# Kernel tuning notes

Hardware: AMD Instinct MI355X
Metric: run time of the kernel (lower is better)

Reference implementation:

```python
import jax, jax.numpy as jnp
import numpy as np

B, D, K = 4096, 768, 60


def setup_inputs() -> dict:
    key = jax.random.key(0)
    k1, k2, k3 = jax.random.split(key, 3)
    user_emb = jax.random.normal(k1, (B, D), dtype=jnp.float32)
    pos_item_emb = jax.random.normal(k2, (B, D), dtype=jnp.float32)
    # Per-row negative indices into the in-batch item table, excluding the
    # row's own positive (emulates the exclusion/sampling done on host in torch).
    r = jax.random.randint(k3, (B, K), 0, B, dtype=jnp.int32)
    rows = jnp.arange(B, dtype=jnp.int32)[:, None]
    neg_indices = jnp.where(r == rows, (r + 1) % B, r)
    return {"user_emb": user_emb, "pos_item_emb": pos_item_emb,
            "neg_indices": neg_indices}


def reference(user_emb, pos_item_emb, neg_indices):
    # u2i contrastive loss: logits = [u.pos, u.neg_1..neg_K], label 0, mean CE.
    logits_pos = jnp.sum(user_emb * pos_item_emb, axis=-1)          # (B,)
    neg_embs = pos_item_emb[neg_indices]                            # (B, K, D)
    logits_neg = jnp.einsum('bd,bkd->bk', user_emb, neg_embs)      # (B, K)
    logits = jnp.concatenate([logits_pos[:, None], logits_neg], axis=1)
    loss = -jax.nn.log_softmax(logits, axis=-1)[:, 0]               # label = 0
    return jnp.mean(loss)
```

## Files before the change

### kernel.cpp

```cpp
#include <hip/hip_runtime.h>
#include <hip/hip_fp16.h>
#include <math.h>


#define NB 4096
#define ND 768
#define NK 60
#define ND4  (ND / 4)
#define NDU  (ND / 2)
#define NLOGITS (NK + 1)
#define NPAD 64

#define NSLOT 64

#define WS_ITEMS_OFF 0
#define WS_USER_OFF  ((size_t)NB * ND * 2)
#define WS_SLOTS_OFF (WS_USER_OFF + (size_t)NB * ND * 2)
#define WS_NEED      (WS_SLOTS_OFF + (size_t)NSLOT * 16 * 4)

typedef _Float16 h2 __attribute__((ext_vector_type(2)));
typedef float    f2 __attribute__((ext_vector_type(2)));
typedef float    f4v __attribute__((ext_vector_type(4)));
typedef unsigned int u4v __attribute__((ext_vector_type(4)));
typedef unsigned int u2v __attribute__((ext_vector_type(2)));

__device__ __forceinline__ float dot2_acc(unsigned int u, unsigned int v, float c) {
#if __has_builtin(__builtin_amdgcn_fdot2)
    return __builtin_amdgcn_fdot2(__builtin_bit_cast(h2, u),
                                  __builtin_bit_cast(h2, v), c, false);
#else
    f2 a = __builtin_convertvector(__builtin_bit_cast(h2, u), f2);
    f2 b = __builtin_convertvector(__builtin_bit_cast(h2, v), f2);
    return c + a.x * b.x + a.y * b.y;
#endif
}

__device__ __forceinline__ unsigned int pack_h2(float x, float y) {
    h2 h = { (_Float16)x, (_Float16)y };
    return __builtin_bit_cast(unsigned int, h);
}

__device__ __forceinline__ float fold8(const float acc[8], int lane) {
    const int bit0 = lane & 1;
    float n[4];
    #pragma unroll
    for (int j = 0; j < 4; ++j) {
        float mine  = bit0 ? acc[2*j+1] : acc[2*j];
        float other = bit0 ? acc[2*j]   : acc[2*j+1];
        n[j] = mine + __shfl_xor(other, 1, 64);
    }
    const int bit1 = (lane >> 1) & 1;
    float s[2];
    #pragma unroll
    for (int j = 0; j < 2; ++j) {
        float mine  = bit1 ? n[2*j+1] : n[2*j];
        float other = bit1 ? n[2*j]   : n[2*j+1];
        s[j] = mine + __shfl_xor(other, 2, 64);
    }
    const int bit2 = (lane >> 2) & 1;
    float mine  = bit2 ? s[1] : s[0];
    float other = bit2 ? s[0] : s[1];
    float r = mine + __shfl_xor(other, 4, 64);
    r += __shfl_xor(r, 8, 64);
    r += __shfl_xor(r, 16, 64);
    r += __shfl_xor(r, 32, 64);
    return r;
}

__global__ __launch_bounds__(256) void convert_all_f16(
    const f4v* __restrict__ items,
    const f4v* __restrict__ user,
    uint2* __restrict__ itemsh,
    uint2* __restrict__ userh,
    float* __restrict__ slots)
{
    const int half = NB * ND4;
    int i = blockIdx.x * 256 + threadIdx.x;

    if (blockIdx.x == 0) {
        ((float4*)slots)[threadIdx.x] = make_float4(0.f, 0.f, 0.f, 0.f);
    }

    const f4v* src = (i < half) ? items : user;
    uint2*     dst = (i < half) ? itemsh : userh;
    int        j   = (i < half) ? i : i - half;

    f4v v = __builtin_nontemporal_load(src + j);
    uint2 rv;
    rv.x = pack_h2(v.x, v.y);
    rv.y = pack_h2(v.z, v.w);
    dst[j] = rv;
}

__global__ __launch_bounds__(512, 8) void gather_lse_fused(
    const unsigned int* __restrict__ userh,
    const unsigned int* __restrict__ itemsh,
    const int* __restrict__ negidx,
    float* __restrict__ slots)
{
    const int tid  = threadIdx.x;
    const int lane = tid & 63;
    const int slot = tid >> 6;
    const int b    = blockIdx.x;

    const int* nrow = negidx + (size_t)b * NK;
    int rows[8];
    #pragma unroll
    for (int i = 0; i < 8; ++i) {
        int k = slot * 8 + i;
        rows[i] = (k == 0 || k > NK) ? b : nrow[k - 1];
    }

    const unsigned int* ur = userh + (size_t)b * NDU;
    uint4 ua = ((const uint4*)ur)[lane];
    uint2 ub = ((const uint2*)(ur + 256))[lane];

    u4v va[8];
    u2v vb[8];
    #pragma unroll
    for (int i = 0; i < 8; ++i) {
        const unsigned int* ir = itemsh + (size_t)rows[i] * NDU;
        va[i] = __builtin_nontemporal_load((const u4v*)ir + lane);
        vb[i] = __builtin_nontemporal_load((const u2v*)(ir + 256) + lane);
    }

    float acc[8];
    #pragma unroll
    for (int i = 0; i < 8; ++i) {
        float a = 0.0f;
        a = dot2_acc(ua.x, va[i].x, a);
        a = dot2_acc(ua.y, va[i].y, a);
        a = dot2_acc(ua.z, va[i].z, a);
        a = dot2_acc(ua.w, va[i].w, a);
        a = dot2_acc(ub.x, vb[i].x, a);
        a = dot2_acc(ub.y, vb[i].y, a);
        acc[i] = a;
    }

    float r = fold8(acc, lane);

    __shared__ float lg[NPAD];
    if (lane < 8)
        lg[slot * 8 + lane] = r;
    __syncthreads();

    if (tid < 64) {
        float v  = (tid < NLOGITS) ? lg[tid] : -INFINITY;
        float p0 = lg[0];
        float m = v;
        #pragma unroll
        for (int off = 32; off > 0; off >>= 1)
            m = fmaxf(m, __shfl_down(m, off, 64));
        m = __shfl(m, 0, 64);
        float e = (tid < NLOGITS) ? __expf(v - m) : 0.0f;
        #pragma unroll
        for (int off = 32; off > 0; off >>= 1)
            e += __shfl_down(e, off, 64);
        if (tid == 0) {
            float loss = m + __logf(e) - p0;
            atomicAdd(&slots[(b & (NSLOT - 1)) * 16], loss);
        }
    }
}

__global__ __launch_bounds__(64) void finish(
    const float* __restrict__ slots, float* __restrict__ out)
{
    const int tid = threadIdx.x;
    float s = slots[tid * 16];
    #pragma unroll
    for (int off = 32; off > 0; off >>= 1)
        s += __shfl_down(s, off, 64);
    if (tid == 0)
        out[0] = s * (1.0f / (float)NB);
}

__global__ __launch_bounds__(256) void u2i_loss_f32(
    const float* __restrict__ user,
    const float* __restrict__ items,
    const int* __restrict__ negidx,
    float* __restrict__ out)
{
    const int b    = blockIdx.x;
    const int tid  = threadIdx.x;
    const int wave = tid >> 6;
    const int lane = tid & 63;

    __shared__ int   rows_s[NPAD];
    __shared__ float logits[NPAD];

    if (tid < NPAD) {
        const int* nrow = negidx + (size_t)b * NK;
        rows_s[tid] = (tid == 0 || tid > NK) ? b : nrow[tid - 1];
    }
    const float4* u4 = (const float4*)user + (size_t)b * ND4;
    float4 u0 = u4[lane];
    float4 u1 = u4[64 + lane];
    float4 u2 = u4[128 + lane];
    __syncthreads();

    const float4* it4 = (const float4*)items;
    #pragma unroll
    for (int j = 0; j < 4; ++j) {
        int ks[4];
        const float4* p[4];
        #pragma unroll
        for (int i = 0; i < 4; ++i) {
            ks[i] = wave + j * 16 + i * 4;
            p[i]  = it4 + (size_t)rows_s[ks[i]] * ND4;
        }
        float4 v0[4], v1[4], v2[4];
        #pragma unroll
        for (int i = 0; i < 4; ++i) {
            v0[i] = p[i][lane];
            v1[i] = p[i][64 + lane];
            v2[i] = p[i][128 + lane];
        }
        float acc[4];
        #pragma unroll
        for (int i = 0; i < 4; ++i) {
            float a;
            a  = u0.x * v0[i].x + u0.y * v0[i].y + u0.z * v0[i].z + u0.w * v0[i].w;
            a += u1.x * v1[i].x + u1.y * v1[i].y + u1.z * v1[i].z + u1.w * v1[i].w;
            a += u2.x * v2[i].x + u2.y * v2[i].y + u2.z * v2[i].z + u2.w * v2[i].w;
            acc[i] = a;
        }
        #pragma unroll
        for (int off = 32; off > 0; off >>= 1) {
            #pragma unroll
            for (int i = 0; i < 4; ++i)
                acc[i] += __shfl_down(acc[i], off, 64);
        }
        if (lane == 0) {
            #pragma unroll
            for (int i = 0; i < 4; ++i)
                logits[ks[i]] = acc[i];
        }
    }
    __syncthreads();

    if (tid < 64) {
        float v = (tid < NLOGITS) ? logits[tid] : -INFINITY;
        float m = v;
        #pragma unroll
        for (int off = 32; off > 0; off >>= 1)
            m = fmaxf(m, __shfl_down(m, off, 64));
        m = __shfl(m, 0, 64);
        float e = (tid < NLOGITS) ? __expf(v - m) : 0.0f;
        #pragma unroll
        for (int off = 32; off > 0; off >>= 1)
            e += __shfl_down(e, off, 64);
        if (tid == 0) {
            float loss = m + __logf(e) - logits[0];
            atomicAdd(out, loss * (1.0f / (float)NB));
        }
    }
}

extern "C" void kernel_launch(void* const* d_in, const int* in_sizes, int n_in,
                              void* d_out, int out_size, void* d_ws, size_t ws_size,
                              hipStream_t stream) {
    const float* user  = (const float*)d_in[0];
    const float* items = (const float*)d_in[1];
    const int*   negi  = (const int*)d_in[2];
    float* out = (float*)d_out;

    if (ws_size >= WS_NEED) {
        char* ws = (char*)d_ws;
        unsigned int* itemsh = (unsigned int*)(ws + WS_ITEMS_OFF);
        unsigned int* userh  = (unsigned int*)(ws + WS_USER_OFF);
        float*        slots  = (float*)(ws + WS_SLOTS_OFF);

        convert_all_f16<<<2 * (NB * ND / 4) / 256, 256, 0, stream>>>(
            (const f4v*)items, (const f4v*)user,
            (uint2*)itemsh, (uint2*)userh, slots);
        gather_lse_fused<<<NB, 512, 0, stream>>>(
            userh, itemsh, negi, slots);
        finish<<<1, 64, 0, stream>>>(slots, out);
    } else {
        hipMemsetAsync(out, 0, sizeof(float), stream);
        u2i_loss_f32<<<NB, 256, 0, stream>>>(user, items, negi, out);
    }
}
```

Measured before the change: 123.3 us.

## Split fp16 item table into three D-planes and gather in three passes

```diff
diff --git a/kernel.cpp b/kernel.cpp
--- a/kernel.cpp
+++ b/kernel.cpp
@@ -7,21 +7,21 @@
 #define ND 768
 #define NK 60
 #define ND4  (ND / 4)
-#define NDU  (ND / 2)
 #define NLOGITS (NK + 1)
 #define NPAD 64
 
 #define NSLOT 64
-
-#define WS_ITEMS_OFF 0
-#define WS_USER_OFF  ((size_t)NB * ND * 2)
-#define WS_SLOTS_OFF (WS_USER_OFF + (size_t)NB * ND * 2)
-#define WS_NEED      (WS_SLOTS_OFF + (size_t)NSLOT * 16 * 4)
+#define PLN_U2 ((size_t)NB * 64)
+
+#define WS_PLANES_OFF 0
+#define WS_USER_OFF   ((size_t)3 * NB * 512)
+#define WS_LOGP_OFF   (WS_USER_OFF + (size_t)NB * ND * 2)
+#define WS_SLOTS_OFF  (WS_LOGP_OFF + (size_t)NB * NPAD * 4)
+#define WS_NEED       (WS_SLOTS_OFF + (size_t)NSLOT * 16 * 4)
 
 typedef _Float16 h2 __attribute__((ext_vector_type(2)));
 typedef float    f2 __attribute__((ext_vector_type(2)));
 typedef float    f4v __attribute__((ext_vector_type(4)));
-typedef unsigned int u4v __attribute__((ext_vector_type(4)));
 typedef unsigned int u2v __attribute__((ext_vector_type(2)));
 
 __device__ __forceinline__ float dot2_acc(unsigned int u, unsigned int v, float c) {
@@ -67,10 +67,10 @@
     return r;
 }
 
-__global__ __launch_bounds__(256) void convert_all_f16(
+__global__ __launch_bounds__(256) void convert_planes(
     const f4v* __restrict__ items,
     const f4v* __restrict__ user,
-    uint2* __restrict__ itemsh,
+    uint2* __restrict__ planes,
     uint2* __restrict__ userh,
     float* __restrict__ slots)
 {
@@ -81,22 +81,32 @@
         ((float4*)slots)[threadIdx.x] = make_float4(0.f, 0.f, 0.f, 0.f);
     }
 
-    const f4v* src = (i < half) ? items : user;
-    uint2*     dst = (i < half) ? itemsh : userh;
-    int        j   = (i < half) ? i : i - half;
-
-    f4v v = __builtin_nontemporal_load(src + j);
-    uint2 rv;
-    rv.x = pack_h2(v.x, v.y);
-    rv.y = pack_h2(v.z, v.w);
-    dst[j] = rv;
-}
-
-__global__ __launch_bounds__(512, 8) void gather_lse_fused(
-    const unsigned int* __restrict__ userh,
-    const unsigned int* __restrict__ itemsh,
+    if (i < half) {
+        f4v v = __builtin_nontemporal_load(items + i);
+        uint2 rv;
+        rv.x = pack_h2(v.x, v.y);
+        rv.y = pack_h2(v.z, v.w);
+        int row = i / ND4;
+        int d4  = i - row * ND4;
+        int p   = d4 >> 6;
+        int off = d4 & 63;
+        planes[(size_t)p * PLN_U2 + (size_t)row * 64 + off] = rv;
+    } else {
+        int j = i - half;
+        f4v v = __builtin_nontemporal_load(user + j);
+        uint2 rv;
+        rv.x = pack_h2(v.x, v.y);
+        rv.y = pack_h2(v.z, v.w);
+        userh[j] = rv;
+    }
+}
+
+template<int P, bool FIRST>
+__global__ __launch_bounds__(512) void gather_pass(
+    const uint2* __restrict__ userh2,
+    const uint2* __restrict__ plane,
     const int* __restrict__ negidx,
-    float* __restrict__ slots)
+    float* __restrict__ logp)
 {
     const int tid  = threadIdx.x;
     const int lane = tid & 63;
@@ -111,37 +121,69 @@
         rows[i] = (k == 0 || k > NK) ? b : nrow[k - 1];
     }
 
-    const unsigned int* ur = userh + (size_t)b * NDU;
-    uint4 ua = ((const uint4*)ur)[lane];
-    uint2 ub = ((const uint2*)(ur + 256))[lane];
-
-    u4v va[8];
-    u2v vb[8];
+    u2v uv = __builtin_nontemporal_load(
+        (const u2v*)(userh2 + (size_t)b * 192 + P * 64) + lane);
+
+    uint2 va[8];
+    #pragma unroll
+    for (int i = 0; i < 8; ++i)
+        va[i] = plane[(size_t)rows[i] * 64 + lane];
+
+    float acc[8];
     #pragma unroll
     for (int i = 0; i < 8; ++i) {
-        const unsigned int* ir = itemsh + (size_t)rows[i] * NDU;
-        va[i] = __builtin_nontemporal_load((const u4v*)ir + lane);
-        vb[i] = __builtin_nontemporal_load((const u2v*)(ir + 256) + lane);
-    }
+        float a = dot2_acc(uv.x, va[i].x, 0.0f);
+        acc[i]  = dot2_acc(uv.y, va[i].y, a);
+    }
+
+    float r = fold8(acc, lane);
+    if (lane < 8) {
+        size_t idx = (size_t)b * NPAD + slot * 8 + lane;
+        logp[idx] = FIRST ? r : logp[idx] + r;
+    }
+}
+
+__global__ __launch_bounds__(512) void gather_pass2_lse(
+    const uint2* __restrict__ userh2,
+    const uint2* __restrict__ plane,
+    const int* __restrict__ negidx,
+    const float* __restrict__ logp,
+    float* __restrict__ slots)
+{
+    const int tid  = threadIdx.x;
+    const int lane = tid & 63;
+    const int slot = tid >> 6;
+    const int b    = blockIdx.x;
+
+    const int* nrow = negidx + (size_t)b * NK;
+    int rows[8];
+    #pragma unroll
+    for (int i = 0; i < 8; ++i) {
+        int k = slot * 8 + i;
+        rows[i] = (k == 0 || k > NK) ? b : nrow[k - 1];
+    }
+
+    u2v uv = __builtin_nontemporal_load(
+        (const u2v*)(userh2 + (size_t)b * 192 + 2 * 64) + lane);
+
+    uint2 va[8];
+    #pragma unroll
+    for (int i = 0; i < 8; ++i)
+        va[i] = plane[(size_t)rows[i] * 64 + lane];
 
     float acc[8];
     #pragma unroll
     for (int i = 0; i < 8; ++i) {
-        float a = 0.0f;
-        a = dot2_acc(ua.x, va[i].x, a);
-        a = dot2_acc(ua.y, va[i].y, a);
-        a = dot2_acc(ua.z, va[i].z, a);
-        a = dot2_acc(ua.w, va[i].w, a);
-        a = dot2_acc(ub.x, vb[i].x, a);
-        a = dot2_acc(ub.y, vb[i].y, a);
-        acc[i] = a;
+        float a = dot2_acc(uv.x, va[i].x, 0.0f);
+        acc[i]  = dot2_acc(uv.y, va[i].y, a);
     }
 
     float r = fold8(acc, lane);
 
     __shared__ float lg[NPAD];
+    float part = logp[(size_t)b * NPAD + slot * 8 + (lane & 7)];
     if (lane < 8)
-        lg[slot * 8 + lane] = r;
+        lg[slot * 8 + lane] = r + part;
     __syncthreads();
 
     if (tid < 64) {
@@ -267,15 +309,19 @@
 
     if (ws_size >= WS_NEED) {
         char* ws = (char*)d_ws;
-        unsigned int* itemsh = (unsigned int*)(ws + WS_ITEMS_OFF);
-        unsigned int* userh  = (unsigned int*)(ws + WS_USER_OFF);
-        float*        slots  = (float*)(ws + WS_SLOTS_OFF);
-
-        convert_all_f16<<<2 * (NB * ND / 4) / 256, 256, 0, stream>>>(
-            (const f4v*)items, (const f4v*)user,
-            (uint2*)itemsh, (uint2*)userh, slots);
-        gather_lse_fused<<<NB, 512, 0, stream>>>(
-            userh, itemsh, negi, slots);
+        uint2* planes = (uint2*)(ws + WS_PLANES_OFF);
+        uint2* userh2 = (uint2*)(ws + WS_USER_OFF);
+        float* logp   = (float*)(ws + WS_LOGP_OFF);
+        float* slots  = (float*)(ws + WS_SLOTS_OFF);
+
+        convert_planes<<<2 * (NB * ND4) / 256, 256, 0, stream>>>(
+            (const f4v*)items, (const f4v*)user, planes, userh2, slots);
+        gather_pass<0, true ><<<NB, 512, 0, stream>>>(
+            userh2, planes,              negi, logp);
+        gather_pass<1, false><<<NB, 512, 0, stream>>>(
+            userh2, planes + PLN_U2,     negi, logp);
+        gather_pass2_lse<<<NB, 512, 0, stream>>>(
+            userh2, planes + 2 * PLN_U2, negi, logp, slots);
         finish<<<1, 64, 0, stream>>>(slots, out);
     } else {
         hipMemsetAsync(out, 0, sizeof(float), stream);
```

After: 119.6 us. 3.0% less time.
